# Optimization experiments

Measured on AMD Instinct MI355X. Metric: run time of the kernel, lower is better.

Reference implementation:

```python
import jax, jax.numpy as jnp
import numpy as np


def setup_inputs() -> dict:
    key = jax.random.key(0)
    B, C, H, W = 8, 64, 64, 64
    x = jax.random.normal(key, (B, C, H, W), dtype=jnp.float32)
    return {"x": x}


def reference(x) -> jnp.ndarray:
    # x: (B, C, H, W). Spatial self-attention over N = H*W positions with
    # Q = K = V = flattened x, no scaling, no projections (the Conv2d in the
    # original __init__ is never used in forward).
    B, C, H, W = x.shape
    N = H * W
    f = x.reshape(B, C, N)  # (B, C, N)
    # att[b, n, m] = sum_c f[b, c, n] * f[b, c, m]  -> (B, N, N)
    att = jnp.einsum('bcn,bcm->bnm', f, f)
    att = jax.nn.softmax(att, axis=-1)
    # outp[b, c, n] = sum_m f[b, c, m] * att[b, n, m]^T  (f_x @ att)
    outp = jnp.einsum('bcm,bmn->bcn', f, att).reshape(B, C, H, W)
    return x + outp
```

## Files before the change

### kernel.cpp

```cpp
#include <hip/hip_runtime.h>

typedef short v8s __attribute__((ext_vector_type(8)));
typedef float v4f __attribute__((ext_vector_type(4)));

#define LOG2E 1.44269504088896340736f

#define WS_FBF_T 0u
#define WS_FVP   4194304u
#define WS_G     8388608u
#define WS_BMAX  8519680u
#define WS_NEED  8521728u

__device__ __forceinline__ unsigned short f2bf_rne(float f) {
  unsigned int u = __builtin_bit_cast(unsigned int, f);
  u += 0x7FFFu + ((u >> 16) & 1u);
  return (unsigned short)(u >> 16);
}

__device__ __forceinline__ unsigned int pack_hi16(float hi, float lo) {
#if defined(__has_builtin) && __has_builtin(__builtin_amdgcn_perm)
  return __builtin_amdgcn_perm(__builtin_bit_cast(unsigned int, hi),
                               __builtin_bit_cast(unsigned int, lo), 0x07060302u);
#else
  return (__builtin_bit_cast(unsigned int, hi) & 0xFFFF0000u) |
         (__builtin_bit_cast(unsigned int, lo) >> 16);
#endif
}

__global__ __launch_bounds__(512) void prep_kernel(
    const float* __restrict__ x, unsigned short* __restrict__ fbf_t,
    unsigned short* __restrict__ fvp, float* __restrict__ g, float* __restrict__ bmax) {
  __shared__ __align__(16) unsigned short T[64 * 66];
  __shared__ float red[8][64];
  const int t = threadIdx.x;
  const int b = blockIdx.x >> 6, ch = blockIdx.x & 63;
  const int n0 = ch << 6, nn = t & 63, cg = t >> 6;

  float sq = 0.f;
#pragma unroll
  for (int j = 0; j < 8; ++j) {
    const int c = cg * 8 + j;
    float v = x[((size_t)(b * 64 + c) << 12) + n0 + nn];
    sq = __builtin_fmaf(v, v, sq);
    T[c * 66 + nn] = f2bf_rne(v);
  }
  red[cg][nn] = sq;
  __syncthreads();

  if (t < 64) {
    float tot = ((red[0][t] + red[1][t]) + (red[2][t] + red[3][t])) +
                ((red[4][t] + red[5][t]) + (red[6][t] + red[7][t]));
    g[b * 4096 + n0 + t] = tot;
    float m = tot;
    m = fmaxf(m, __shfl_xor(m, 1, 64));
    m = fmaxf(m, __shfl_xor(m, 2, 64));
    m = fmaxf(m, __shfl_xor(m, 4, 64));
    m = fmaxf(m, __shfl_xor(m, 8, 64));
    m = fmaxf(m, __shfl_xor(m, 16, 64));
    m = fmaxf(m, __shfl_xor(m, 32, 64));
    if (t == 0) bmax[b * 64 + ch] = m;
  }

  {
    const int nt = t >> 3, q8 = t & 7;
    unsigned short u[8];
#pragma unroll
    for (int j = 0; j < 8; ++j) u[j] = T[(q8 * 8 + j) * 66 + nt];
    *(v8s*)&fbf_t[((size_t)b << 18) + (size_t)(n0 + nt) * 64 + q8 * 8] = *(v8s*)u;
  }

  {
    const int c = t >> 3, s8 = t & 7;
    const int base = c * 66 + ((s8 >> 2) << 5) + ((s8 & 3) << 2);
    unsigned int w0 = *(const unsigned int*)&T[base];
    unsigned int w1 = *(const unsigned int*)&T[base + 2];
    unsigned int w2 = *(const unsigned int*)&T[base + 16];
    unsigned int w3 = *(const unsigned int*)&T[base + 18];
    uint4 uu;
    uu.x = w0; uu.y = w1; uu.z = w2; uu.w = w3;
    *(uint4*)&fvp[((size_t)(b * 64 + c) << 12) + n0 + s8 * 8] = uu;
  }
}

#define QKPV(JQ, AK, AV)                                                        \
  {                                                                             \
    v4f s0 = (v4f){0.f, 0.f, 0.f, 0.f}, s1 = (v4f){0.f, 0.f, 0.f, 0.f};         \
    _Pragma("unroll")                                                           \
    for (int cs = 0; cs < 2; ++cs) {                                            \
      s0 = __builtin_amdgcn_mfma_f32_16x16x32_bf16(AK[0][cs], bQ[JQ][cs], s0,   \
                                                   0, 0, 0);                    \
      s1 = __builtin_amdgcn_mfma_f32_16x16x32_bf16(AK[1][cs], bQ[JQ][cs], s1,   \
                                                   0, 0, 0);                    \
    }                                                                           \
    float p0[4], p1[4];                                                         \
    _Pragma("unroll")                                                           \
    for (int r = 0; r < 4; ++r) {                                               \
      p0[r] = __builtin_amdgcn_exp2f(__builtin_fmaf(s0[r], LOG2E, -msc[JQ]));   \
      p1[r] = __builtin_amdgcn_exp2f(__builtin_fmaf(s1[r], LOG2E, -msc[JQ]));   \
    }                                                                           \
    rsum[JQ] += ((p0[0] + p0[1]) + (p0[2] + p0[3])) +                           \
                ((p1[0] + p1[1]) + (p1[2] + p1[3]));                            \
    uint4 up;                                                                   \
    up.x = pack_hi16(p0[1], p0[0]);                                             \
    up.y = pack_hi16(p0[3], p0[2]);                                             \
    up.z = pack_hi16(p1[1], p1[0]);                                             \
    up.w = pack_hi16(p1[3], p1[2]);                                             \
    v8s bp = __builtin_bit_cast(v8s, up);                                       \
    _Pragma("unroll")                                                           \
    for (int ct = 0; ct < 4; ++ct)                                              \
      oacc[ct][JQ] = __builtin_amdgcn_mfma_f32_16x16x32_bf16(AV[ct], bp,        \
                                                             oacc[ct][JQ],      \
                                                             0, 0, 0);          \
  }

__global__ __launch_bounds__(512, 2) void chanattn_main(
    const float* __restrict__ x, const unsigned short* __restrict__ fbf_t,
    const unsigned short* __restrict__ fvp, const float* __restrict__ g,
    const float* __restrict__ bmax, float* __restrict__ out) {
  __shared__ __align__(16) unsigned char smem[143360];
  unsigned short* sKtB = (unsigned short*)smem;
  unsigned short* sVcB = (unsigned short*)(smem + 36864);
  float* lred = (float*)(smem + 141312);
  const int PAIR = 35328;

  const int tid = threadIdx.x;
  const int wave = tid >> 6, lane = tid & 63, quad = lane >> 4, l15 = lane & 15;
  const int qg = wave >> 2, kg = wave & 3;
  const int b = blockIdx.x >> 5, qt = blockIdx.x & 31;

  const unsigned short* fT = fbf_t + ((size_t)b << 18);
  const unsigned short* fV = fvp + ((size_t)b << 18);

  const int sKey = tid >> 3, sC = (tid & 7) << 3;
  const int vC = tid >> 4, vK = (tid & 15) << 3;

  float gm = bmax[b * 64 + lane];
  gm = fmaxf(gm, __shfl_xor(gm, 1, 64));
  gm = fmaxf(gm, __shfl_xor(gm, 2, 64));
  gm = fmaxf(gm, __shfl_xor(gm, 4, 64));
  gm = fmaxf(gm, __shfl_xor(gm, 8, 64));
  gm = fmaxf(gm, __shfl_xor(gm, 16, 64));
  gm = fmaxf(gm, __shfl_xor(gm, 32, 64));
  float gq[4];
#pragma unroll
  for (int jq = 0; jq < 4; ++jq)
    gq[jq] = g[b * 4096 + qt * 128 + qg * 64 + jq * 16 + l15];

#pragma unroll
  for (int i = 0; i < 2; ++i)
    *(v8s*)&sKtB[(sKey + i * 64) * 72 + sC] =
        *(const v8s*)&fT[(size_t)(qt * 128 + sKey + i * 64) * 64 + sC];
  v8s pfk[4], pfv[4];
#pragma unroll
  for (int i = 0; i < 4; ++i)
    pfk[i] = *(const v8s*)&fT[(size_t)(sKey + i * 64) * 64 + sC];
#pragma unroll
  for (int i2 = 0; i2 < 2; ++i2)
#pragma unroll
    for (int j = 0; j < 2; ++j)
      pfv[i2 * 2 + j] = *(const v8s*)&fV[(size_t)(vC + i2 * 32) * 4096 + vK + j * 128];

  __syncthreads();
  v8s bQ[4][2];
#pragma unroll
  for (int jq = 0; jq < 4; ++jq)
#pragma unroll
    for (int cs = 0; cs < 2; ++cs)
      bQ[jq][cs] = *(const v8s*)&sKtB[(qg * 64 + jq * 16 + l15) * 72 + cs * 32 + quad * 8];
  float msc[4];
#pragma unroll
  for (int jq = 0; jq < 4; ++jq) msc[jq] = __builtin_sqrtf(gq[jq] * gm) * LOG2E;
  __syncthreads();

#pragma unroll
  for (int i = 0; i < 4; ++i)
    *(v8s*)&sKtB[(sKey + i * 64) * 72 + sC] = pfk[i];
#pragma unroll
  for (int i2 = 0; i2 < 2; ++i2)
#pragma unroll
    for (int j = 0; j < 2; ++j)
      *(v8s*)&sVcB[(vC + i2 * 32) * 264 + vK + j * 128] = pfv[i2 * 2 + j];
#pragma unroll
  for (int i = 0; i < 4; ++i)
    pfk[i] = *(const v8s*)&fT[(size_t)(256 + sKey + i * 64) * 64 + sC];
#pragma unroll
  for (int i2 = 0; i2 < 2; ++i2)
#pragma unroll
    for (int j = 0; j < 2; ++j)
      pfv[i2 * 2 + j] =
          *(const v8s*)&fV[(size_t)(vC + i2 * 32) * 4096 + 256 + vK + j * 128];

  v4f oacc[4][4];
  float rsum[4];
#pragma unroll
  for (int ct = 0; ct < 4; ++ct)
#pragma unroll
    for (int jq = 0; jq < 4; ++jq) oacc[ct][jq] = (v4f){0.f, 0.f, 0.f, 0.f};
#pragma unroll
  for (int jq = 0; jq < 4; ++jq) rsum[jq] = 0.f;

  for (int kt = 0; kt < 16; ++kt) {
    __syncthreads();
    const int po = (kt & 1) * PAIR;
    const int pn = po ^ PAIR;

    v8s aK[2][2];
#pragma unroll
    for (int t = 0; t < 2; ++t)
#pragma unroll
      for (int cs = 0; cs < 2; ++cs)
        aK[t][cs] =
            *(const v8s*)&sKtB[po + (kg * 64 + t * 16 + l15) * 72 + cs * 32 + quad * 8];
    v8s aV[4];
#pragma unroll
    for (int ct = 0; ct < 4; ++ct)
      aV[ct] = *(const v8s*)&sVcB[po + (ct * 16 + l15) * 264 + kg * 64 + quad * 8];

    QKPV(0, aK, aV);

    if (kt < 15) {
#pragma unroll
      for (int i = 0; i < 4; ++i)
        *(v8s*)&sKtB[pn + (sKey + i * 64) * 72 + sC] = pfk[i];
#pragma unroll
      for (int i2 = 0; i2 < 2; ++i2)
#pragma unroll
        for (int j = 0; j < 2; ++j)
          *(v8s*)&sVcB[pn + (vC + i2 * 32) * 264 + vK + j * 128] = pfv[i2 * 2 + j];
    }
    if (kt < 14) {
      const int k0 = (kt + 2) << 8;
#pragma unroll
      for (int i = 0; i < 4; ++i)
        pfk[i] = *(const v8s*)&fT[(size_t)(k0 + sKey + i * 64) * 64 + sC];
#pragma unroll
      for (int i2 = 0; i2 < 2; ++i2)
#pragma unroll
        for (int j = 0; j < 2; ++j)
          pfv[i2 * 2 + j] =
              *(const v8s*)&fV[(size_t)(vC + i2 * 32) * 4096 + k0 + vK + j * 128];
    }

#pragma unroll
    for (int jq = 1; jq < 4; ++jq) QKPV(jq, aK, aV);

    v8s aK1[2][2];
#pragma unroll
    for (int t = 0; t < 2; ++t)
#pragma unroll
      for (int cs = 0; cs < 2; ++cs)
        aK1[t][cs] = *(const v8s*)&sKtB[po + (kg * 64 + 32 + t * 16 + l15) * 72 +
                                        cs * 32 + quad * 8];
    v8s aV1[4];
#pragma unroll
    for (int ct = 0; ct < 4; ++ct)
      aV1[ct] =
          *(const v8s*)&sVcB[po + (ct * 16 + l15) * 264 + kg * 64 + 32 + quad * 8];

#pragma unroll
    for (int jq = 0; jq < 4; ++jq) QKPV(jq, aK1, aV1);
  }

#pragma unroll
  for (int jq = 0; jq < 4; ++jq) {
    float s = rsum[jq];
    s += __shfl_xor(s, 16, 64);
    s += __shfl_xor(s, 32, 64);
    rsum[jq] = s;
  }
  if (quad == 0) {
#pragma unroll
    for (int jq = 0; jq < 4; ++jq)
      lred[(qg * 64 + jq * 16 + l15) * 4 + kg] = rsum[jq];
  }
  __syncthreads();
  float inv[4];
#pragma unroll
  for (int jq = 0; jq < 4; ++jq) {
    const float4 lv = *(const float4*)&lred[(qg * 64 + jq * 16 + l15) * 4];
    inv[jq] = __builtin_amdgcn_rcpf((lv.x + lv.y) + (lv.z + lv.w));
  }

  float* Obuf = (float*)smem;
#pragma unroll
  for (int round = 0; round < 4; ++round) {
    if (kg == round) {
#pragma unroll
      for (int ct = 0; ct < 4; ++ct)
#pragma unroll
        for (int jq = 0; jq < 4; ++jq)
#pragma unroll
          for (int r = 0; r < 4; ++r) {
            float val = oacc[ct][jq][r] * inv[jq];
            float* p = &Obuf[(qg * 64 + ct * 16 + quad * 4 + r) * 68 + jq * 16 + l15];
            if (round == 0) *p = val; else *p += val;
          }
    }
    __syncthreads();
  }
#pragma unroll
  for (int j = 0; j < 4; ++j) {
    int idx = tid + j * 512;
    int qg2 = idx >> 10, c = (idx >> 4) & 63, q4 = idx & 15;
    const float4 o = *(const float4*)&Obuf[(qg2 * 64 + c) * 68 + q4 * 4];
    size_t gidx = ((size_t)(b * 64 + c) << 12) + (unsigned)(qt * 128 + qg2 * 64 + q4 * 4);
    const float4 xv = *(const float4*)(x + gidx);
    float4 rv;
    rv.x = xv.x + o.x; rv.y = xv.y + o.y; rv.z = xv.z + o.z; rv.w = xv.w + o.w;
    *(float4*)(out + gidx) = rv;
  }
}

__global__ __launch_bounds__(512) void
chanattn_fallback(const float* __restrict__ x, float* __restrict__ out) {
  __shared__ __align__(16) unsigned char smem[54272];
  unsigned short* sKt = (unsigned short*)smem;
  unsigned short* sVc = (unsigned short*)(smem + 18432);
  unsigned short* sP  = (unsigned short*)(smem + 35840);
  const int tid = threadIdx.x;
  const int wave = tid >> 6, lane = tid & 63, quad = lane >> 4, l15 = lane & 15;
  const int b = blockIdx.x & 7, qt = blockIdx.x >> 3;
  const float* fb = x + (size_t)b * (64 * 4096);
  const int skey = tid & 127, sc0 = (tid >> 7) << 4;
  {
    float vq[16];
#pragma unroll
    for (int j = 0; j < 16; ++j) vq[j] = fb[(sc0 + j) * 4096 + qt * 128 + skey];
    unsigned short us[16];
#pragma unroll
    for (int j = 0; j < 16; ++j) us[j] = f2bf_rne(vq[j]);
#pragma unroll
    for (int h = 0; h < 2; ++h) {
      v8s t;
#pragma unroll
      for (int j = 0; j < 8; ++j) t[j] = (short)us[h * 8 + j];
      *(v8s*)&sKt[skey * 72 + sc0 + h * 8] = t;
    }
  }
  float vk[16];
#pragma unroll
  for (int j = 0; j < 16; ++j) vk[j] = fb[(sc0 + j) * 4096 + skey];
  __syncthreads();
  v8s aq[2];
#pragma unroll
  for (int cs = 0; cs < 2; ++cs)
    aq[cs] = *(const v8s*)&sKt[(wave * 16 + l15) * 72 + cs * 32 + quad * 8];
  __syncthreads();
  v4f oacc[4];
#pragma unroll
  for (int ct = 0; ct < 4; ++ct) oacc[ct] = (v4f){0.f, 0.f, 0.f, 0.f};
  float m_run[4], l_run[4];
#pragma unroll
  for (int r = 0; r < 4; ++r) { m_run[r] = -3.0e38f; l_run[r] = 0.f; }
  unsigned short* sPw = sP + wave * (16 * 72);
  for (int kt = 0; kt < 32; ++kt) {
    {
      unsigned short us[16];
#pragma unroll
      for (int j = 0; j < 16; ++j) us[j] = f2bf_rne(vk[j]);
#pragma unroll
      for (int h = 0; h < 2; ++h) {
        v8s t;
#pragma unroll
        for (int j = 0; j < 8; ++j) t[j] = (short)us[h * 8 + j];
        *(v8s*)&sKt[skey * 72 + sc0 + h * 8] = t;
      }
#pragma unroll
      for (int j = 0; j < 16; ++j) sVc[(sc0 + j) * 136 + skey] = us[j];
    }
    __syncthreads();
    if (kt + 1 < 32) {
      const int m0 = (kt + 1) * 128;
#pragma unroll
      for (int j = 0; j < 16; ++j) vk[j] = fb[(sc0 + j) * 4096 + m0 + skey];
    }
    v4f sacc[8];
#pragma unroll
    for (int t = 0; t < 8; ++t) {
      v4f acc = (v4f){0.f, 0.f, 0.f, 0.f};
#pragma unroll
      for (int cs = 0; cs < 2; ++cs) {
        v8s bf = *(const v8s*)&sKt[(t * 16 + l15) * 72 + cs * 32 + quad * 8];
        acc = __builtin_amdgcn_mfma_f32_16x16x32_bf16(aq[cs], bf, acc, 0, 0, 0);
      }
      sacc[t] = acc;
    }
    float alpha[4], msc[4], rsum[4];
#pragma unroll
    for (int r = 0; r < 4; ++r) {
      float mv = sacc[0][r];
#pragma unroll
      for (int t = 1; t < 8; ++t) mv = fmaxf(mv, sacc[t][r]);
      mv = fmaxf(mv, __shfl_xor(mv, 8, 64));
      mv = fmaxf(mv, __shfl_xor(mv, 4, 64));
      mv = fmaxf(mv, __shfl_xor(mv, 2, 64));
      mv = fmaxf(mv, __shfl_xor(mv, 1, 64));
      float mnew = fmaxf(m_run[r], mv);
      alpha[r] = __builtin_amdgcn_exp2f((m_run[r] - mnew) * LOG2E);
      m_run[r] = mnew;
      msc[r] = mnew * LOG2E;
      l_run[r] *= alpha[r];
      rsum[r] = 0.f;
    }
#pragma unroll
    for (int ct = 0; ct < 4; ++ct)
#pragma unroll
      for (int r = 0; r < 4; ++r) oacc[ct][r] *= alpha[r];
#pragma unroll
    for (int half = 0; half < 2; ++half) {
#pragma unroll
      for (int t = half * 4; t < half * 4 + 4; ++t)
#pragma unroll
        for (int r = 0; r < 4; ++r) {
          float p = __builtin_amdgcn_exp2f(__builtin_fmaf(sacc[t][r], LOG2E, -msc[r]));
          rsum[r] += p;
          sPw[(quad * 4 + r) * 72 + (t - half * 4) * 16 + l15] = f2bf_rne(p);
        }
      asm volatile("s_waitcnt lgkmcnt(0)" ::: "memory");
#pragma unroll
      for (int ms = 0; ms < 2; ++ms) {
        v8s af = *(const v8s*)&sPw[l15 * 72 + ms * 32 + quad * 8];
#pragma unroll
        for (int ct = 0; ct < 4; ++ct) {
          v8s bf = *(const v8s*)&sVc[(ct * 16 + l15) * 136 + (half * 2 + ms) * 32 + quad * 8];
          oacc[ct] = __builtin_amdgcn_mfma_f32_16x16x32_bf16(af, bf, oacc[ct], 0, 0, 0);
        }
      }
      asm volatile("s_waitcnt lgkmcnt(0)" ::: "memory");
    }
#pragma unroll
    for (int r = 0; r < 4; ++r) {
      float s = rsum[r];
      s += __shfl_xor(s, 8, 64);
      s += __shfl_xor(s, 4, 64);
      s += __shfl_xor(s, 2, 64);
      s += __shfl_xor(s, 1, 64);
      l_run[r] += s;
    }
    __syncthreads();
  }
  float inv[4];
#pragma unroll
  for (int r = 0; r < 4; ++r) inv[r] = __builtin_amdgcn_rcpf(l_run[r]);
  float* sOt = (float*)smem;
#pragma unroll
  for (int ct = 0; ct < 4; ++ct)
#pragma unroll
    for (int r = 0; r < 4; ++r)
      sOt[(ct * 16 + l15) * 132 + wave * 16 + quad * 4 + r] = oacc[ct][r] * inv[r];
  __syncthreads();
#pragma unroll
  for (int j = 0; j < 4; ++j) {
    int idx = tid + j * 512;
    int nv = idx & 31, c = idx >> 5;
    float4 o = *(const float4*)&sOt[c * 132 + nv * 4];
    size_t gaddr = (size_t)b * (64 * 4096) + (size_t)c * 4096 + (size_t)(qt * 128 + nv * 4);
    float4 xv = *(const float4*)(x + gaddr);
    float4 res = make_float4(xv.x + o.x, xv.y + o.y, xv.z + o.z, xv.w + o.w);
    *(float4*)(out + gaddr) = res;
  }
}

extern "C" void kernel_launch(void* const* d_in, const int* in_sizes, int n_in,
                              void* d_out, int out_size, void* d_ws, size_t ws_size,
                              hipStream_t stream) {
  const float* xin = (const float*)d_in[0];
  float* out = (float*)d_out;
  if (ws_size >= (size_t)WS_NEED) {
    unsigned short* fbf_t = (unsigned short*)((char*)d_ws + WS_FBF_T);
    unsigned short* fvp = (unsigned short*)((char*)d_ws + WS_FVP);
    float* g = (float*)((char*)d_ws + WS_G);
    float* bmax = (float*)((char*)d_ws + WS_BMAX);
    prep_kernel<<<dim3(512), dim3(512), 0, stream>>>(xin, fbf_t, fvp, g, bmax);
    chanattn_main<<<dim3(256), dim3(512), 0, stream>>>(xin, fbf_t, fvp, g, bmax, out);
  } else {
    chanattn_fallback<<<dim3(256), dim3(512), 0, stream>>>(xin, out);
  }
}
```

Baseline: 101.3 us.

## Load K/V MFMA fragments directly from global memory, drop LDS staging

Removes the double-buffered LDS staging of K and V tiles and the per-iteration barriers. Each wave now loads its MFMA operand fragments straight from global memory (L2/L1) into registers, using a two-stage register ping-pong prefetch. This cuts LDS traffic, barriers and shared memory size, which may raise occupancy. The cost is more global/L2 loads, since waves that share K/V tiles no longer share them through LDS, and exposed memory latency.

```diff
diff --git a/kernel.cpp b/kernel.cpp
--- a/kernel.cpp
+++ b/kernel.cpp
@@ -113,15 +113,34 @@
                                                              0, 0, 0);          \
   }
 
+#define LOADH(BUF, KT, KS)                                                      \
+  {                                                                             \
+    const size_t ko = (size_t)((KT) * 256 + (KS) * 32);                         \
+    BUF[0] = *(const v8s*)&pK[ko * 64];                                         \
+    BUF[1] = *(const v8s*)&pK[ko * 64 + 32];                                    \
+    BUF[2] = *(const v8s*)&pK[(ko + 16) * 64];                                  \
+    BUF[3] = *(const v8s*)&pK[(ko + 16) * 64 + 32];                             \
+    BUF[4] = *(const v8s*)&pV[ko];                                              \
+    BUF[5] = *(const v8s*)&pV[65536 + ko];                                      \
+    BUF[6] = *(const v8s*)&pV[131072 + ko];                                     \
+    BUF[7] = *(const v8s*)&pV[196608 + ko];                                     \
+  }
+
+#define COMPUTEH(BUF)                                                           \
+  {                                                                             \
+    v8s aK_[2][2] = {{BUF[0], BUF[1]}, {BUF[2], BUF[3]}};                       \
+    v8s aV_[4] = {BUF[4], BUF[5], BUF[6], BUF[7]};                              \
+    _Pragma("unroll")                                                           \
+    for (int jq = 0; jq < 4; ++jq) QKPV(jq, aK_, aV_);                          \
+  }
+
 __global__ __launch_bounds__(512, 2) void chanattn_main(
     const float* __restrict__ x, const unsigned short* __restrict__ fbf_t,
     const unsigned short* __restrict__ fvp, const float* __restrict__ g,
     const float* __restrict__ bmax, float* __restrict__ out) {
-  __shared__ __align__(16) unsigned char smem[143360];
-  unsigned short* sKtB = (unsigned short*)smem;
-  unsigned short* sVcB = (unsigned short*)(smem + 36864);
-  float* lred = (float*)(smem + 141312);
-  const int PAIR = 35328;
+  __shared__ __align__(16) unsigned char smem[36864];
+  float* Obuf = (float*)smem;
+  float* lred = (float*)(smem + 34816);
 
   const int tid = threadIdx.x;
   const int wave = tid >> 6, lane = tid & 63, quad = lane >> 4, l15 = lane & 15;
@@ -130,9 +149,6 @@
 
   const unsigned short* fT = fbf_t + ((size_t)b << 18);
   const unsigned short* fV = fvp + ((size_t)b << 18);
-
-  const int sKey = tid >> 3, sC = (tid & 7) << 3;
-  const int vC = tid >> 4, vK = (tid & 15) << 3;
 
   float gm = bmax[b * 64 + lane];
   gm = fmaxf(gm, __shfl_xor(gm, 1, 64));
@@ -146,49 +162,19 @@
   for (int jq = 0; jq < 4; ++jq)
     gq[jq] = g[b * 4096 + qt * 128 + qg * 64 + jq * 16 + l15];
 
-#pragma unroll
-  for (int i = 0; i < 2; ++i)
-    *(v8s*)&sKtB[(sKey + i * 64) * 72 + sC] =
-        *(const v8s*)&fT[(size_t)(qt * 128 + sKey + i * 64) * 64 + sC];
-  v8s pfk[4], pfv[4];
-#pragma unroll
-  for (int i = 0; i < 4; ++i)
-    pfk[i] = *(const v8s*)&fT[(size_t)(sKey + i * 64) * 64 + sC];
-#pragma unroll
-  for (int i2 = 0; i2 < 2; ++i2)
-#pragma unroll
-    for (int j = 0; j < 2; ++j)
-      pfv[i2 * 2 + j] = *(const v8s*)&fV[(size_t)(vC + i2 * 32) * 4096 + vK + j * 128];
-
-  __syncthreads();
   v8s bQ[4][2];
 #pragma unroll
   for (int jq = 0; jq < 4; ++jq)
 #pragma unroll
     for (int cs = 0; cs < 2; ++cs)
-      bQ[jq][cs] = *(const v8s*)&sKtB[(qg * 64 + jq * 16 + l15) * 72 + cs * 32 + quad * 8];
+      bQ[jq][cs] = *(const v8s*)&fT[(size_t)(qt * 128 + qg * 64 + jq * 16 + l15) * 64 +
+                                    cs * 32 + quad * 8];
   float msc[4];
 #pragma unroll
   for (int jq = 0; jq < 4; ++jq) msc[jq] = __builtin_sqrtf(gq[jq] * gm) * LOG2E;
-  __syncthreads();
-
-#pragma unroll
-  for (int i = 0; i < 4; ++i)
-    *(v8s*)&sKtB[(sKey + i * 64) * 72 + sC] = pfk[i];
-#pragma unroll
-  for (int i2 = 0; i2 < 2; ++i2)
-#pragma unroll
-    for (int j = 0; j < 2; ++j)
-      *(v8s*)&sVcB[(vC + i2 * 32) * 264 + vK + j * 128] = pfv[i2 * 2 + j];
-#pragma unroll
-  for (int i = 0; i < 4; ++i)
-    pfk[i] = *(const v8s*)&fT[(size_t)(256 + sKey + i * 64) * 64 + sC];
-#pragma unroll
-  for (int i2 = 0; i2 < 2; ++i2)
-#pragma unroll
-    for (int j = 0; j < 2; ++j)
-      pfv[i2 * 2 + j] =
-          *(const v8s*)&fV[(size_t)(vC + i2 * 32) * 4096 + 256 + vK + j * 128];
+
+  const unsigned short* pK = fT + (size_t)(kg * 64 + l15) * 64 + quad * 8;
+  const unsigned short* pV = fV + (size_t)l15 * 4096 + kg * 64 + quad * 8;
 
   v4f oacc[4][4];
   float rsum[4];
@@ -199,66 +185,13 @@
 #pragma unroll
   for (int jq = 0; jq < 4; ++jq) rsum[jq] = 0.f;
 
+  v8s A[8], Bf[8];
+  LOADH(A, 0, 0);
   for (int kt = 0; kt < 16; ++kt) {
-    __syncthreads();
-    const int po = (kt & 1) * PAIR;
-    const int pn = po ^ PAIR;
-
-    v8s aK[2][2];
-#pragma unroll
-    for (int t = 0; t < 2; ++t)
-#pragma unroll
-      for (int cs = 0; cs < 2; ++cs)
-        aK[t][cs] =
-            *(const v8s*)&sKtB[po + (kg * 64 + t * 16 + l15) * 72 + cs * 32 + quad * 8];
-    v8s aV[4];
-#pragma unroll
-    for (int ct = 0; ct < 4; ++ct)
-      aV[ct] = *(const v8s*)&sVcB[po + (ct * 16 + l15) * 264 + kg * 64 + quad * 8];
-
-    QKPV(0, aK, aV);
-
-    if (kt < 15) {
-#pragma unroll
-      for (int i = 0; i < 4; ++i)
-        *(v8s*)&sKtB[pn + (sKey + i * 64) * 72 + sC] = pfk[i];
-#pragma unroll
-      for (int i2 = 0; i2 < 2; ++i2)
-#pragma unroll
-        for (int j = 0; j < 2; ++j)
-          *(v8s*)&sVcB[pn + (vC + i2 * 32) * 264 + vK + j * 128] = pfv[i2 * 2 + j];
-    }
-    if (kt < 14) {
-      const int k0 = (kt + 2) << 8;
-#pragma unroll
-      for (int i = 0; i < 4; ++i)
-        pfk[i] = *(const v8s*)&fT[(size_t)(k0 + sKey + i * 64) * 64 + sC];
-#pragma unroll
-      for (int i2 = 0; i2 < 2; ++i2)
-#pragma unroll
-        for (int j = 0; j < 2; ++j)
-          pfv[i2 * 2 + j] =
-              *(const v8s*)&fV[(size_t)(vC + i2 * 32) * 4096 + k0 + vK + j * 128];
-    }
-
-#pragma unroll
-    for (int jq = 1; jq < 4; ++jq) QKPV(jq, aK, aV);
-
-    v8s aK1[2][2];
-#pragma unroll
-    for (int t = 0; t < 2; ++t)
-#pragma unroll
-      for (int cs = 0; cs < 2; ++cs)
-        aK1[t][cs] = *(const v8s*)&sKtB[po + (kg * 64 + 32 + t * 16 + l15) * 72 +
-                                        cs * 32 + quad * 8];
-    v8s aV1[4];
-#pragma unroll
-    for (int ct = 0; ct < 4; ++ct)
-      aV1[ct] =
-          *(const v8s*)&sVcB[po + (ct * 16 + l15) * 264 + kg * 64 + 32 + quad * 8];
-
-#pragma unroll
-    for (int jq = 0; jq < 4; ++jq) QKPV(jq, aK1, aV1);
+    LOADH(Bf, kt, 1);
+    COMPUTEH(A);
+    if (kt < 15) LOADH(A, kt + 1, 0);
+    COMPUTEH(Bf);
   }
 
 #pragma unroll
@@ -281,7 +214,6 @@
     inv[jq] = __builtin_amdgcn_rcpf((lv.x + lv.y) + (lv.z + lv.w));
   }
 
-  float* Obuf = (float*)smem;
 #pragma unroll
   for (int round = 0; round < 4; ++round) {
     if (kg == round) {
```

Measured after the change: 126.3 us. +24.6%, slower.

## Halve query tile per block, single-buffer LDS, launch twice as many blocks

Applied to the files above, without the earlier changes.

Each block now handles 64 queries instead of 128, with all 8 waves splitting the 256-key tile into 32-key slices, and the grid doubles to 512 blocks. The K/V shared-memory tiles drop from double to single buffering, with two barriers per iteration. This roughly halves shared memory so up to four blocks can fit per CU, and Q is read straight from global memory into registers. In exchange, each block re-reads the full K/V stream, so global and L2 traffic doubles, and the extra barriers plus the reduction of two partial outputs add synchronisation cost.

```diff
diff --git a/kernel.cpp b/kernel.cpp
--- a/kernel.cpp
+++ b/kernel.cpp
@@ -113,20 +113,21 @@
                                                              0, 0, 0);          \
   }
 
-__global__ __launch_bounds__(512, 2) void chanattn_main(
+__global__ __launch_bounds__(512, 4) void chanattn_main(
     const float* __restrict__ x, const unsigned short* __restrict__ fbf_t,
     const unsigned short* __restrict__ fvp, const float* __restrict__ g,
     const float* __restrict__ bmax, float* __restrict__ out) {
-  __shared__ __align__(16) unsigned char smem[143360];
-  unsigned short* sKtB = (unsigned short*)smem;
-  unsigned short* sVcB = (unsigned short*)(smem + 36864);
-  float* lred = (float*)(smem + 141312);
-  const int PAIR = 35328;
+  __shared__ __align__(16) unsigned char smem[72704];
+  unsigned short* sKt = (unsigned short*)smem;
+  unsigned short* sVc = (unsigned short*)(smem + 36864);
+  float* lred = (float*)(smem + 70656);
+  float* OA = (float*)smem;
+  float* OB = (float*)(smem + 17408);
 
   const int tid = threadIdx.x;
   const int wave = tid >> 6, lane = tid & 63, quad = lane >> 4, l15 = lane & 15;
-  const int qg = wave >> 2, kg = wave & 3;
-  const int b = blockIdx.x >> 5, qt = blockIdx.x & 31;
+  const int kg = wave;
+  const int b = blockIdx.x >> 6, qt = blockIdx.x & 63;
 
   const unsigned short* fT = fbf_t + ((size_t)b << 18);
   const unsigned short* fV = fvp + ((size_t)b << 18);
@@ -144,12 +145,19 @@
   float gq[4];
 #pragma unroll
   for (int jq = 0; jq < 4; ++jq)
-    gq[jq] = g[b * 4096 + qt * 128 + qg * 64 + jq * 16 + l15];
-
-#pragma unroll
-  for (int i = 0; i < 2; ++i)
-    *(v8s*)&sKtB[(sKey + i * 64) * 72 + sC] =
-        *(const v8s*)&fT[(size_t)(qt * 128 + sKey + i * 64) * 64 + sC];
+    gq[jq] = g[b * 4096 + qt * 64 + jq * 16 + l15];
+
+  v8s bQ[4][2];
+#pragma unroll
+  for (int jq = 0; jq < 4; ++jq)
+#pragma unroll
+    for (int cs = 0; cs < 2; ++cs)
+      bQ[jq][cs] = *(const v8s*)&fT[(size_t)(qt * 64 + jq * 16 + l15) * 64 +
+                                    cs * 32 + quad * 8];
+  float msc[4];
+#pragma unroll
+  for (int jq = 0; jq < 4; ++jq) msc[jq] = __builtin_sqrtf(gq[jq] * gm) * LOG2E;
+
   v8s pfk[4], pfv[4];
 #pragma unroll
   for (int i = 0; i < 4; ++i)
@@ -159,27 +167,14 @@
 #pragma unroll
     for (int j = 0; j < 2; ++j)
       pfv[i2 * 2 + j] = *(const v8s*)&fV[(size_t)(vC + i2 * 32) * 4096 + vK + j * 128];
-
-  __syncthreads();
-  v8s bQ[4][2];
-#pragma unroll
-  for (int jq = 0; jq < 4; ++jq)
-#pragma unroll
-    for (int cs = 0; cs < 2; ++cs)
-      bQ[jq][cs] = *(const v8s*)&sKtB[(qg * 64 + jq * 16 + l15) * 72 + cs * 32 + quad * 8];
-  float msc[4];
-#pragma unroll
-  for (int jq = 0; jq < 4; ++jq) msc[jq] = __builtin_sqrtf(gq[jq] * gm) * LOG2E;
-  __syncthreads();
-
 #pragma unroll
   for (int i = 0; i < 4; ++i)
-    *(v8s*)&sKtB[(sKey + i * 64) * 72 + sC] = pfk[i];
+    *(v8s*)&sKt[(sKey + i * 64) * 72 + sC] = pfk[i];
 #pragma unroll
   for (int i2 = 0; i2 < 2; ++i2)
 #pragma unroll
     for (int j = 0; j < 2; ++j)
-      *(v8s*)&sVcB[(vC + i2 * 32) * 264 + vK + j * 128] = pfv[i2 * 2 + j];
+      *(v8s*)&sVc[(vC + i2 * 32) * 264 + vK + j * 128] = pfv[i2 * 2 + j];
 #pragma unroll
   for (int i = 0; i < 4; ++i)
     pfk[i] = *(const v8s*)&fT[(size_t)(256 + sKey + i * 64) * 64 + sC];
@@ -199,34 +194,32 @@
 #pragma unroll
   for (int jq = 0; jq < 4; ++jq) rsum[jq] = 0.f;
 
+  __syncthreads();
+
   for (int kt = 0; kt < 16; ++kt) {
-    __syncthreads();
-    const int po = (kt & 1) * PAIR;
-    const int pn = po ^ PAIR;
-
     v8s aK[2][2];
 #pragma unroll
     for (int t = 0; t < 2; ++t)
 #pragma unroll
       for (int cs = 0; cs < 2; ++cs)
         aK[t][cs] =
-            *(const v8s*)&sKtB[po + (kg * 64 + t * 16 + l15) * 72 + cs * 32 + quad * 8];
+            *(const v8s*)&sKt[(kg * 32 + t * 16 + l15) * 72 + cs * 32 + quad * 8];
     v8s aV[4];
 #pragma unroll
     for (int ct = 0; ct < 4; ++ct)
-      aV[ct] = *(const v8s*)&sVcB[po + (ct * 16 + l15) * 264 + kg * 64 + quad * 8];
-
-    QKPV(0, aK, aV);
+      aV[ct] = *(const v8s*)&sVc[(ct * 16 + l15) * 264 + kg * 32 + quad * 8];
+
+    __syncthreads();
 
     if (kt < 15) {
 #pragma unroll
       for (int i = 0; i < 4; ++i)
-        *(v8s*)&sKtB[pn + (sKey + i * 64) * 72 + sC] = pfk[i];
+        *(v8s*)&sKt[(sKey + i * 64) * 72 + sC] = pfk[i];
 #pragma unroll
       for (int i2 = 0; i2 < 2; ++i2)
 #pragma unroll
         for (int j = 0; j < 2; ++j)
-          *(v8s*)&sVcB[pn + (vC + i2 * 32) * 264 + vK + j * 128] = pfv[i2 * 2 + j];
+          *(v8s*)&sVc[(vC + i2 * 32) * 264 + vK + j * 128] = pfv[i2 * 2 + j];
     }
     if (kt < 14) {
       const int k0 = (kt + 2) << 8;
@@ -242,23 +235,9 @@
     }
 
 #pragma unroll
-    for (int jq = 1; jq < 4; ++jq) QKPV(jq, aK, aV);
-
-    v8s aK1[2][2];
-#pragma unroll
-    for (int t = 0; t < 2; ++t)
-#pragma unroll
-      for (int cs = 0; cs < 2; ++cs)
-        aK1[t][cs] = *(const v8s*)&sKtB[po + (kg * 64 + 32 + t * 16 + l15) * 72 +
-                                        cs * 32 + quad * 8];
-    v8s aV1[4];
-#pragma unroll
-    for (int ct = 0; ct < 4; ++ct)
-      aV1[ct] =
-          *(const v8s*)&sVcB[po + (ct * 16 + l15) * 264 + kg * 64 + 32 + quad * 8];
-
-#pragma unroll
-    for (int jq = 0; jq < 4; ++jq) QKPV(jq, aK1, aV1);
+    for (int jq = 0; jq < 4; ++jq) QKPV(jq, aK, aV);
+
+    __syncthreads();
   }
 
 #pragma unroll
@@ -271,20 +250,23 @@
   if (quad == 0) {
 #pragma unroll
     for (int jq = 0; jq < 4; ++jq)
-      lred[(qg * 64 + jq * 16 + l15) * 4 + kg] = rsum[jq];
+      lred[(jq * 16 + l15) * 8 + kg] = rsum[jq];
   }
   __syncthreads();
   float inv[4];
 #pragma unroll
   for (int jq = 0; jq < 4; ++jq) {
-    const float4 lv = *(const float4*)&lred[(qg * 64 + jq * 16 + l15) * 4];
-    inv[jq] = __builtin_amdgcn_rcpf((lv.x + lv.y) + (lv.z + lv.w));
-  }
-
-  float* Obuf = (float*)smem;
+    const float4 lv0 = *(const float4*)&lred[(jq * 16 + l15) * 8];
+    const float4 lv1 = *(const float4*)&lred[(jq * 16 + l15) * 8 + 4];
+    inv[jq] = __builtin_amdgcn_rcpf(((lv0.x + lv0.y) + (lv0.z + lv0.w)) +
+                                    ((lv1.x + lv1.y) + (lv1.z + lv1.w)));
+  }
+  __syncthreads();
+
 #pragma unroll
   for (int round = 0; round < 4; ++round) {
-    if (kg == round) {
+    if ((kg & 3) == round) {
+      float* O = (kg < 4) ? OA : OB;
 #pragma unroll
       for (int ct = 0; ct < 4; ++ct)
 #pragma unroll
@@ -292,21 +274,26 @@
 #pragma unroll
           for (int r = 0; r < 4; ++r) {
             float val = oacc[ct][jq][r] * inv[jq];
-            float* p = &Obuf[(qg * 64 + ct * 16 + quad * 4 + r) * 68 + jq * 16 + l15];
+            float* p = &O[(ct * 16 + quad * 4 + r) * 68 + jq * 16 + l15];
             if (round == 0) *p = val; else *p += val;
           }
     }
     __syncthreads();
   }
-#pragma unroll
-  for (int j = 0; j < 4; ++j) {
+
+#pragma unroll
+  for (int j = 0; j < 2; ++j) {
     int idx = tid + j * 512;
-    int qg2 = idx >> 10, c = (idx >> 4) & 63, q4 = idx & 15;
-    const float4 o = *(const float4*)&Obuf[(qg2 * 64 + c) * 68 + q4 * 4];
-    size_t gidx = ((size_t)(b * 64 + c) << 12) + (unsigned)(qt * 128 + qg2 * 64 + q4 * 4);
+    int c = idx >> 4, q4 = idx & 15;
+    const float4 oa = *(const float4*)&OA[c * 68 + q4 * 4];
+    const float4 ob = *(const float4*)&OB[c * 68 + q4 * 4];
+    size_t gidx = ((size_t)(b * 64 + c) << 12) + (unsigned)(qt * 64 + q4 * 4);
     const float4 xv = *(const float4*)(x + gidx);
     float4 rv;
-    rv.x = xv.x + o.x; rv.y = xv.y + o.y; rv.z = xv.z + o.z; rv.w = xv.w + o.w;
+    rv.x = xv.x + oa.x + ob.x;
+    rv.y = xv.y + oa.y + ob.y;
+    rv.z = xv.z + oa.z + ob.z;
+    rv.w = xv.w + oa.w + ob.w;
     *(float4*)(out + gidx) = rv;
   }
 }
@@ -472,7 +459,7 @@
     float* g = (float*)((char*)d_ws + WS_G);
     float* bmax = (float*)((char*)d_ws + WS_BMAX);
     prep_kernel<<<dim3(512), dim3(512), 0, stream>>>(xin, fbf_t, fvp, g, bmax);
-    chanattn_main<<<dim3(256), dim3(512), 0, stream>>>(xin, fbf_t, fvp, g, bmax, out);
+    chanattn_main<<<dim3(512), dim3(512), 0, stream>>>(xin, fbf_t, fvp, g, bmax, out);
   } else {
     chanattn_fallback<<<dim3(256), dim3(512), 0, stream>>>(xin, out);
   }
```

New measurement: 378.3 us. 3.73x slower.

## Double waves per block by splitting key tiles across eight wave groups

Applied to the files above, without the earlier changes.

Raises the main kernel's block from 512 to 1024 threads, so each query group spreads every 256-key tile over 8 waves of 32 keys instead of 4 waves of 64 keys. This halves per-wave MFMA work per iteration and the per-thread prefetch registers, aiming for more latency hiding inside one block per CU. Q fragments now come straight from global memory instead of staging through LDS with two barriers. The price is a longer 8-round serialized output reduction through shared memory, plus an extra barrier, and launch_bounds(1024) caps registers per thread.

```diff
diff --git a/kernel.cpp b/kernel.cpp
--- a/kernel.cpp
+++ b/kernel.cpp
@@ -113,19 +113,19 @@
                                                              0, 0, 0);          \
   }
 
-__global__ __launch_bounds__(512, 2) void chanattn_main(
+__global__ __launch_bounds__(1024) void chanattn_main(
     const float* __restrict__ x, const unsigned short* __restrict__ fbf_t,
     const unsigned short* __restrict__ fvp, const float* __restrict__ g,
     const float* __restrict__ bmax, float* __restrict__ out) {
-  __shared__ __align__(16) unsigned char smem[143360];
-  unsigned short* sKtB = (unsigned short*)smem;
-  unsigned short* sVcB = (unsigned short*)(smem + 36864);
+  __shared__ __align__(16) unsigned char smem[145408];
+  unsigned short* sKt = (unsigned short*)smem;
+  unsigned short* sVc = (unsigned short*)(smem + 36864);
   float* lred = (float*)(smem + 141312);
   const int PAIR = 35328;
 
   const int tid = threadIdx.x;
   const int wave = tid >> 6, lane = tid & 63, quad = lane >> 4, l15 = lane & 15;
-  const int qg = wave >> 2, kg = wave & 3;
+  const int qg = wave >> 3, kg = wave & 7;
   const int b = blockIdx.x >> 5, qt = blockIdx.x & 31;
 
   const unsigned short* fT = fbf_t + ((size_t)b << 18);
@@ -146,49 +146,36 @@
   for (int jq = 0; jq < 4; ++jq)
     gq[jq] = g[b * 4096 + qt * 128 + qg * 64 + jq * 16 + l15];
 
+  v8s bQ[4][2];
+#pragma unroll
+  for (int jq = 0; jq < 4; ++jq)
+#pragma unroll
+    for (int cs = 0; cs < 2; ++cs)
+      bQ[jq][cs] = *(const v8s*)&fT[(size_t)(qt * 128 + qg * 64 + jq * 16 + l15) * 64 +
+                                    cs * 32 + quad * 8];
+  float msc[4];
+#pragma unroll
+  for (int jq = 0; jq < 4; ++jq) msc[jq] = __builtin_sqrtf(gq[jq] * gm) * LOG2E;
+
+  v8s pfk[2], pfv[2];
 #pragma unroll
   for (int i = 0; i < 2; ++i)
-    *(v8s*)&sKtB[(sKey + i * 64) * 72 + sC] =
-        *(const v8s*)&fT[(size_t)(qt * 128 + sKey + i * 64) * 64 + sC];
-  v8s pfk[4], pfv[4];
-#pragma unroll
-  for (int i = 0; i < 4; ++i)
-    pfk[i] = *(const v8s*)&fT[(size_t)(sKey + i * 64) * 64 + sC];
-#pragma unroll
-  for (int i2 = 0; i2 < 2; ++i2)
-#pragma unroll
-    for (int j = 0; j < 2; ++j)
-      pfv[i2 * 2 + j] = *(const v8s*)&fV[(size_t)(vC + i2 * 32) * 4096 + vK + j * 128];
-
-  __syncthreads();
-  v8s bQ[4][2];
-#pragma unroll
-  for (int jq = 0; jq < 4; ++jq)
-#pragma unroll
-    for (int cs = 0; cs < 2; ++cs)
-      bQ[jq][cs] = *(const v8s*)&sKtB[(qg * 64 + jq * 16 + l15) * 72 + cs * 32 + quad * 8];
-  float msc[4];
-#pragma unroll
-  for (int jq = 0; jq < 4; ++jq) msc[jq] = __builtin_sqrtf(gq[jq] * gm) * LOG2E;
-  __syncthreads();
-
-#pragma unroll
-  for (int i = 0; i < 4; ++i)
-    *(v8s*)&sKtB[(sKey + i * 64) * 72 + sC] = pfk[i];
-#pragma unroll
-  for (int i2 = 0; i2 < 2; ++i2)
-#pragma unroll
-    for (int j = 0; j < 2; ++j)
-      *(v8s*)&sVcB[(vC + i2 * 32) * 264 + vK + j * 128] = pfv[i2 * 2 + j];
-#pragma unroll
-  for (int i = 0; i < 4; ++i)
-    pfk[i] = *(const v8s*)&fT[(size_t)(256 + sKey + i * 64) * 64 + sC];
-#pragma unroll
-  for (int i2 = 0; i2 < 2; ++i2)
-#pragma unroll
-    for (int j = 0; j < 2; ++j)
-      pfv[i2 * 2 + j] =
-          *(const v8s*)&fV[(size_t)(vC + i2 * 32) * 4096 + 256 + vK + j * 128];
+    pfk[i] = *(const v8s*)&fT[(size_t)(sKey + i * 128) * 64 + sC];
+#pragma unroll
+  for (int j = 0; j < 2; ++j)
+    pfv[j] = *(const v8s*)&fV[(size_t)vC * 4096 + vK + j * 128];
+#pragma unroll
+  for (int i = 0; i < 2; ++i)
+    *(v8s*)&sKt[(sKey + i * 128) * 72 + sC] = pfk[i];
+#pragma unroll
+  for (int j = 0; j < 2; ++j)
+    *(v8s*)&sVc[vC * 264 + vK + j * 128] = pfv[j];
+#pragma unroll
+  for (int i = 0; i < 2; ++i)
+    pfk[i] = *(const v8s*)&fT[(size_t)(256 + sKey + i * 128) * 64 + sC];
+#pragma unroll
+  for (int j = 0; j < 2; ++j)
+    pfv[j] = *(const v8s*)&fV[(size_t)vC * 4096 + 256 + vK + j * 128];
 
   v4f oacc[4][4];
   float rsum[4];
@@ -210,55 +197,34 @@
 #pragma unroll
       for (int cs = 0; cs < 2; ++cs)
         aK[t][cs] =
-            *(const v8s*)&sKtB[po + (kg * 64 + t * 16 + l15) * 72 + cs * 32 + quad * 8];
+            *(const v8s*)&sKt[po + (kg * 32 + t * 16 + l15) * 72 + cs * 32 + quad * 8];
     v8s aV[4];
 #pragma unroll
     for (int ct = 0; ct < 4; ++ct)
-      aV[ct] = *(const v8s*)&sVcB[po + (ct * 16 + l15) * 264 + kg * 64 + quad * 8];
+      aV[ct] = *(const v8s*)&sVc[po + (ct * 16 + l15) * 264 + kg * 32 + quad * 8];
 
     QKPV(0, aK, aV);
 
     if (kt < 15) {
 #pragma unroll
-      for (int i = 0; i < 4; ++i)
-        *(v8s*)&sKtB[pn + (sKey + i * 64) * 72 + sC] = pfk[i];
-#pragma unroll
-      for (int i2 = 0; i2 < 2; ++i2)
-#pragma unroll
-        for (int j = 0; j < 2; ++j)
-          *(v8s*)&sVcB[pn + (vC + i2 * 32) * 264 + vK + j * 128] = pfv[i2 * 2 + j];
+      for (int i = 0; i < 2; ++i)
+        *(v8s*)&sKt[pn + (sKey + i * 128) * 72 + sC] = pfk[i];
+#pragma unroll
+      for (int j = 0; j < 2; ++j)
+        *(v8s*)&sVc[pn + vC * 264 + vK + j * 128] = pfv[j];
     }
     if (kt < 14) {
       const int k0 = (kt + 2) << 8;
 #pragma unroll
-      for (int i = 0; i < 4; ++i)
-        pfk[i] = *(const v8s*)&fT[(size_t)(k0 + sKey + i * 64) * 64 + sC];
-#pragma unroll
-      for (int i2 = 0; i2 < 2; ++i2)
-#pragma unroll
-        for (int j = 0; j < 2; ++j)
-          pfv[i2 * 2 + j] =
-              *(const v8s*)&fV[(size_t)(vC + i2 * 32) * 4096 + k0 + vK + j * 128];
+      for (int i = 0; i < 2; ++i)
+        pfk[i] = *(const v8s*)&fT[(size_t)(k0 + sKey + i * 128) * 64 + sC];
+#pragma unroll
+      for (int j = 0; j < 2; ++j)
+        pfv[j] = *(const v8s*)&fV[(size_t)vC * 4096 + k0 + vK + j * 128];
     }
 
 #pragma unroll
     for (int jq = 1; jq < 4; ++jq) QKPV(jq, aK, aV);
-
-    v8s aK1[2][2];
-#pragma unroll
-    for (int t = 0; t < 2; ++t)
-#pragma unroll
-      for (int cs = 0; cs < 2; ++cs)
-        aK1[t][cs] = *(const v8s*)&sKtB[po + (kg * 64 + 32 + t * 16 + l15) * 72 +
-                                        cs * 32 + quad * 8];
-    v8s aV1[4];
-#pragma unroll
-    for (int ct = 0; ct < 4; ++ct)
-      aV1[ct] =
-          *(const v8s*)&sVcB[po + (ct * 16 + l15) * 264 + kg * 64 + 32 + quad * 8];
-
-#pragma unroll
-    for (int jq = 0; jq < 4; ++jq) QKPV(jq, aK1, aV1);
   }
 
 #pragma unroll
@@ -271,19 +237,22 @@
   if (quad == 0) {
 #pragma unroll
     for (int jq = 0; jq < 4; ++jq)
-      lred[(qg * 64 + jq * 16 + l15) * 4 + kg] = rsum[jq];
+      lred[(qg * 64 + jq * 16 + l15) * 8 + kg] = rsum[jq];
   }
   __syncthreads();
   float inv[4];
 #pragma unroll
   for (int jq = 0; jq < 4; ++jq) {
-    const float4 lv = *(const float4*)&lred[(qg * 64 + jq * 16 + l15) * 4];
-    inv[jq] = __builtin_amdgcn_rcpf((lv.x + lv.y) + (lv.z + lv.w));
-  }
+    const float4 lv0 = *(const float4*)&lred[(qg * 64 + jq * 16 + l15) * 8];
+    const float4 lv1 = *(const float4*)&lred[(qg * 64 + jq * 16 + l15) * 8 + 4];
+    inv[jq] = __builtin_amdgcn_rcpf(((lv0.x + lv0.y) + (lv0.z + lv0.w)) +
+                                    ((lv1.x + lv1.y) + (lv1.z + lv1.w)));
+  }
+  __syncthreads();
 
   float* Obuf = (float*)smem;
 #pragma unroll
-  for (int round = 0; round < 4; ++round) {
+  for (int round = 0; round < 8; ++round) {
     if (kg == round) {
 #pragma unroll
       for (int ct = 0; ct < 4; ++ct)
@@ -299,8 +268,8 @@
     __syncthreads();
   }
 #pragma unroll
-  for (int j = 0; j < 4; ++j) {
-    int idx = tid + j * 512;
+  for (int j = 0; j < 2; ++j) {
+    int idx = tid + j * 1024;
     int qg2 = idx >> 10, c = (idx >> 4) & 63, q4 = idx & 15;
     const float4 o = *(const float4*)&Obuf[(qg2 * 64 + c) * 68 + q4 * 4];
     size_t gidx = ((size_t)(b * 64 + c) << 12) + (unsigned)(qt * 128 + qg2 * 64 + q4 * 4);
@@ -472,7 +441,7 @@
     float* g = (float*)((char*)d_ws + WS_G);
     float* bmax = (float*)((char*)d_ws + WS_BMAX);
     prep_kernel<<<dim3(512), dim3(512), 0, stream>>>(xin, fbf_t, fvp, g, bmax);
-    chanattn_main<<<dim3(256), dim3(512), 0, stream>>>(xin, fbf_t, fvp, g, bmax, out);
+    chanattn_main<<<dim3(256), dim3(1024), 0, stream>>>(xin, fbf_t, fvp, g, bmax, out);
   } else {
     chanattn_fallback<<<dim3(256), dim3(512), 0, stream>>>(xin, out);
   }
```

Measured after the change: 256.6 us. +153.3%, slower.
